# Optimization experiments

Measured on AMD Instinct MI355X. Metric: run time of the kernel, lower is better.

Reference implementation:

```python
import jax, jax.numpy as jnp
import numpy as np

B, SQ, SK, D, H = 8, 2048, 2048, 512, 8
QP, KP, VP = 512, 512, 4096  # VP must equal D*H for O_w to accept the concat


def setup_inputs() -> dict:
    key = jax.random.key(0)
    ks = jax.random.split(key, 9)
    q_in = jax.random.normal(ks[0], (B, SQ, D), dtype=jnp.float32)
    k_in = jax.random.normal(ks[1], (B, SK, D), dtype=jnp.float32)
    v_in = jax.random.normal(ks[2], (B, SK, D), dtype=jnp.float32)
    mask = jax.random.randint(ks[3], (B, SQ, SK), 0, 2, dtype=jnp.int32)
    W_q = jax.random.normal(ks[4], (D, QP), dtype=jnp.float32) * 0.02
    W_k = jax.random.normal(ks[5], (D, KP), dtype=jnp.float32) * 0.02
    W_v = jax.random.normal(ks[6], (D, VP), dtype=jnp.float32) * 0.02
    W_o = jax.random.normal(ks[7], (VP, D), dtype=jnp.float32) * 0.02
    b_o = jnp.zeros((D,), dtype=jnp.float32)
    return {"q_in": q_in, "k_in": k_in, "v_in": v_in,
            "W_q": W_q, "W_k": W_k, "W_v": W_v, "W_o": W_o, "b_o": b_o,
            "mask": mask}


def reference(q_in, k_in, v_in, W_q, W_k, W_v, W_o, b_o, mask):
    b, sq, d = q_in.shape
    sk = k_in.shape[1]
    # NOTE: original scales by sqrt(input_dim // num_heads), NOT actual head dim
    scale = jnp.asarray(np.sqrt(d // H), dtype=q_in.dtype)
    q = q_in @ W_q  # (B, Sq, QP)
    k = k_in @ W_k  # (B, Sk, KP)
    v = v_in @ W_v  # (B, Sk, VP)
    q_h = q.reshape(b, sq, H, -1).transpose(0, 2, 1, 3)  # (B,H,Sq,dq)
    k_h = k.reshape(b, sk, H, -1).transpose(0, 2, 1, 3)  # (B,H,Sk,dk)
    v_h = v.reshape(b, sk, H, -1).transpose(0, 2, 1, 3)  # (B,H,Sk,dv)
    attn = jnp.einsum('bhid,bhkd->bhik', q_h, k_h)  # (B,H,Sq,Sk)
    attn = jnp.where(mask[:, None, :, :] == 0, jnp.asarray(-1e9, attn.dtype), attn)
    attn = jax.nn.softmax(attn / scale, axis=-1)
    out = attn @ v_h  # (B,H,Sq,dv)
    # Faithful to original bug: transpose(0,1) swaps BATCH and HEAD, then reshape
    out = jnp.transpose(out, (1, 0, 2, 3)).reshape(b, sq, -1)  # (B,Sq,H*dv)
    return out @ W_o + b_o
```

## Files before the change

kernel.cpp:

```cpp
#include <hip/hip_runtime.h>
#include <math.h>

typedef __bf16 bf16x8 __attribute__((ext_vector_type(8)));
typedef float fx4 __attribute__((ext_vector_type(4)));
typedef unsigned short u16;
typedef unsigned short u16x8 __attribute__((ext_vector_type(8)));
typedef unsigned int u32;

__device__ __forceinline__ fx4 mfma16(bf16x8 a, bf16x8 b, fx4 c) {
  return __builtin_amdgcn_mfma_f32_16x16x32_bf16(a, b, c, 0, 0, 0);
}
__device__ __forceinline__ u16 f2bf(float f) {
  u32 u = __float_as_uint(f);
  u += 0x7fffu + ((u >> 16) & 1u);
  return (u16)(u >> 16);
}

#define BB 8
#define SS 2048
#define DD 512
#define HH 8
#define DQ 64
#define DV 512
#define VP 4096

#define OFF_QP  ((size_t)0)
#define OFF_KP  ((size_t)16777216)
#define OFF_WQT ((size_t)33554432)
#define OFF_WKT ((size_t)34078720)
#define OFF_WVT ((size_t)34603008)
#define OFF_WOT ((size_t)38797312)
#define OFF_VT  ((size_t)76546048)
#define OFF_XB  ((size_t)210763776)

__global__ __launch_bounds__(256) void transpose_w(const float* __restrict__ W,
                                                   u16* __restrict__ Wt,
                                                   int K, int N) {
  __shared__ float t[32][33];
  const int n0 = blockIdx.x * 32, k0 = blockIdx.y * 32;
  const int tx = threadIdx.x & 31, ty = threadIdx.x >> 5;
#pragma unroll
  for (int i = 0; i < 32; i += 8)
    t[ty + i][tx] = W[(size_t)(k0 + ty + i) * N + n0 + tx];
  __syncthreads();
#pragma unroll
  for (int i = 0; i < 32; i += 8)
    Wt[(size_t)(n0 + ty + i) * K + k0 + tx] = f2bf(t[tx][ty + i]);
}

template <int AFP32, int EPI>
__global__ __launch_bounds__(256) void gemm_bt(const void* __restrict__ Ap,
                                               const u16* __restrict__ Bt,
                                               void* __restrict__ Cp,
                                               int M, int N, int K,
                                               const float* __restrict__ bias,
                                               float scale) {
  __shared__ union {
    struct { u16 As[128 * 32]; u16 Bs[128 * 32]; } s;
    u16 T[4][64 * 68];
  } sm;
  const int tid = threadIdx.x;
  const int lane = tid & 63, w = tid >> 6;
  const int lhi = lane >> 4, llo = lane & 15;
  const int wm = w >> 1, wn = w & 1;
  const int m0 = blockIdx.y * 128, n0 = blockIdx.x * 128;

  fx4 acc[4][4];
#pragma unroll
  for (int i = 0; i < 4; ++i)
#pragma unroll
    for (int j = 0; j < 4; ++j) acc[i][j] = (fx4){0.f, 0.f, 0.f, 0.f};

  for (int k0 = 0; k0 < K; k0 += 32) {
    if (AFP32) {
      const float* A = (const float*)Ap;
      const int row = tid >> 1, co = (tid & 1) * 16;
      const float* src = A + (size_t)(m0 + row) * K + k0 + co;
      float4 v0 = *(const float4*)(src + 0);
      float4 v1 = *(const float4*)(src + 4);
      float4 v2 = *(const float4*)(src + 8);
      float4 v3 = *(const float4*)(src + 12);
      u16x8 p0 = {f2bf(v0.x), f2bf(v0.y), f2bf(v0.z), f2bf(v0.w),
                  f2bf(v1.x), f2bf(v1.y), f2bf(v1.z), f2bf(v1.w)};
      u16x8 p1 = {f2bf(v2.x), f2bf(v2.y), f2bf(v2.z), f2bf(v2.w),
                  f2bf(v3.x), f2bf(v3.y), f2bf(v3.z), f2bf(v3.w)};
      *(u16x8*)&sm.s.As[row * 32 + co] = p0;
      *(u16x8*)&sm.s.As[row * 32 + co + 8] = p1;
    } else {
      const u16* A = (const u16*)Ap;
#pragma unroll
      for (int j = 0; j < 2; ++j) {
        int cc = j * 256 + tid;
        int row = cc >> 2, c8 = (cc & 3) * 8;
        *(uint4*)&sm.s.As[cc * 8] = *(const uint4*)&A[(size_t)(m0 + row) * K + k0 + c8];
      }
    }
#pragma unroll
    for (int j = 0; j < 2; ++j) {
      int cc = j * 256 + tid;
      int row = cc >> 2, c8 = (cc & 3) * 8;
      *(uint4*)&sm.s.Bs[cc * 8] = *(const uint4*)&Bt[(size_t)(n0 + row) * K + k0 + c8];
    }
    __syncthreads();
    bf16x8 af[4], bfv[4];
#pragma unroll
    for (int mi = 0; mi < 4; ++mi)
      af[mi] = *(const bf16x8*)&sm.s.As[(wm * 64 + mi * 16 + llo) * 32 + lhi * 8];
#pragma unroll
    for (int ni = 0; ni < 4; ++ni)
      bfv[ni] = *(const bf16x8*)&sm.s.Bs[(wn * 64 + ni * 16 + llo) * 32 + lhi * 8];
#pragma unroll
    for (int mi = 0; mi < 4; ++mi)
#pragma unroll
      for (int ni = 0; ni < 4; ++ni)
        acc[mi][ni] = mfma16(af[mi], bfv[ni], acc[mi][ni]);
    __syncthreads();
  }

  const int rbase = m0 + wm * 64, cbase = n0 + wn * 64;
  if (EPI == 0) {
    u16* C = (u16*)Cp;
#pragma unroll
    for (int mi = 0; mi < 4; ++mi) {
      int r0 = rbase + mi * 16 + lhi * 4;
#pragma unroll
      for (int ni = 0; ni < 4; ++ni) {
        int c = cbase + ni * 16 + llo;
#pragma unroll
        for (int r = 0; r < 4; ++r)
          C[(size_t)(r0 + r) * N + c] = f2bf(acc[mi][ni][r] * scale);
      }
    }
  } else if (EPI == 1) {
    u16* Tw = &sm.T[w][0];
#pragma unroll
    for (int mi = 0; mi < 4; ++mi)
#pragma unroll
      for (int ni = 0; ni < 4; ++ni) {
        ushort4 pk;
        pk.x = f2bf(acc[mi][ni][0]);
        pk.y = f2bf(acc[mi][ni][1]);
        pk.z = f2bf(acc[mi][ni][2]);
        pk.w = f2bf(acc[mi][ni][3]);
        *(ushort4*)&Tw[(ni * 16 + llo) * 68 + mi * 16 + lhi * 4] = pk;
      }
    u16* VtC = (u16*)Cp;
    const int bsel = rbase >> 11;
    const int sb = rbase & 2047;
    u16* dst = VtC + ((size_t)(bsel * VP + cbase + lane)) * SS + sb;
#pragma unroll
    for (int j = 0; j < 8; ++j) {
      u16x8 vv = *(u16x8*)&Tw[lane * 68 + j * 8];
      *(u16x8*)&dst[j * 8] = vv;
    }
  } else {
    float* C = (float*)Cp;
#pragma unroll
    for (int ni = 0; ni < 4; ++ni) {
      int c = cbase + ni * 16 + llo;
      float bv = bias[c];
#pragma unroll
      for (int mi = 0; mi < 4; ++mi) {
        int r0 = rbase + mi * 16 + lhi * 4;
#pragma unroll
        for (int r = 0; r < 4; ++r)
          C[(size_t)(r0 + r) * N + c] = acc[mi][ni][r] + bv;
      }
    }
  }
}

#define SM_S 68
__global__ __launch_bounds__(256, 2) void attn(const u16* __restrict__ Qp,
                                               const u16* __restrict__ Kp,
                                               const u16* __restrict__ Vt,
                                               const int* __restrict__ mask,
                                               u16* __restrict__ Xb) {
  const int lin = blockIdx.x;
  const int xcd = lin & 7, idx = lin >> 3;
  const int bh = xcd * 8 + (idx >> 5);
  const int qt = idx & 31;
  const int b = bh & 7, h = bh >> 3;
  const int m0 = qt * 64;
  const int tid = threadIdx.x, w = tid >> 6, lane = tid & 63;
  const int lhi = lane >> 4, llo = lane & 15;

  __shared__ float Ssm[64 * SM_S];
  __shared__ u16 Psm[64 * SM_S];
  __shared__ float sm_l[64];

  bf16x8 qf[4][2];
#pragma unroll
  for (int mt = 0; mt < 4; ++mt)
#pragma unroll
    for (int ks = 0; ks < 2; ++ks)
      qf[mt][ks] = *(const bf16x8*)&Qp[(size_t)(b * SS + m0 + mt * 16 + llo) * 512 +
                                       h * DQ + ks * 32 + lhi * 8];

  fx4 acc[4][8];
#pragma unroll
  for (int mt = 0; mt < 4; ++mt)
#pragma unroll
    for (int nt = 0; nt < 8; ++nt) acc[mt][nt] = (fx4){0.f, 0.f, 0.f, 0.f};

  const int r8 = tid >> 3, c8 = (tid & 7) * 8;
  const int* mrow0 = mask + (size_t)(b * SS + m0 + r8) * SS;
  const int* mrow1 = mrow0 + 32 * SS;
  float ls0 = 0.f, ls1 = 0.f;

  const int colw = w * 16 + llo;
  const size_t kbase = (size_t)(b * SS) * 512 + h * DQ + lhi * 8;

  for (int n0 = 0; n0 < SS; n0 += 64) {
    bf16x8 kf0 = *(const bf16x8*)&Kp[kbase + (size_t)(n0 + colw) * 512];
    bf16x8 kf1 = *(const bf16x8*)&Kp[kbase + (size_t)(n0 + colw) * 512 + 32];
    int4 ma0 = *(const int4*)&mrow0[n0 + c8];
    int4 ma1 = *(const int4*)&mrow0[n0 + c8 + 4];
    int4 mb0 = *(const int4*)&mrow1[n0 + c8];
    int4 mb1 = *(const int4*)&mrow1[n0 + c8 + 4];

#pragma unroll
    for (int mt = 0; mt < 4; ++mt) {
      fx4 s = (fx4){0.f, 0.f, 0.f, 0.f};
      s = mfma16(qf[mt][0], kf0, s);
      s = mfma16(qf[mt][1], kf1, s);
#pragma unroll
      for (int r = 0; r < 4; ++r)
        Ssm[(mt * 16 + lhi * 4 + r) * SM_S + colw] = s[r];
    }
    __syncthreads();

#pragma unroll
    for (int half = 0; half < 2; ++half) {
      const int rr = r8 + half * 32;
      const int4 mv0 = half ? mb0 : ma0;
      const int4 mv1 = half ? mb1 : ma1;
      float4 xa = *(const float4*)&Ssm[rr * SM_S + c8];
      float4 xb = *(const float4*)&Ssm[rr * SM_S + c8 + 4];
      float x0 = mv0.x ? xa.x : -1.25e8f;
      float x1 = mv0.y ? xa.y : -1.25e8f;
      float x2 = mv0.z ? xa.z : -1.25e8f;
      float x3 = mv0.w ? xa.w : -1.25e8f;
      float x4 = mv1.x ? xb.x : -1.25e8f;
      float x5 = mv1.y ? xb.y : -1.25e8f;
      float x6 = mv1.z ? xb.z : -1.25e8f;
      float x7 = mv1.w ? xb.w : -1.25e8f;
      float p0 = __expf(x0), p1 = __expf(x1), p2 = __expf(x2), p3 = __expf(x3);
      float p4 = __expf(x4), p5 = __expf(x5), p6 = __expf(x6), p7 = __expf(x7);
      u16x8 pb = {f2bf(p0), f2bf(p1), f2bf(p2), f2bf(p3),
                  f2bf(p4), f2bf(p5), f2bf(p6), f2bf(p7)};
      *(u16x8*)&Psm[rr * SM_S + c8] = pb;
      float ps = ((p0 + p1) + (p2 + p3)) + ((p4 + p5) + (p6 + p7));
      if (half) ls1 += ps; else ls0 += ps;
    }
    __syncthreads();

    bf16x8 pf[4][2];
#pragma unroll
    for (int mt = 0; mt < 4; ++mt)
#pragma unroll
      for (int kk = 0; kk < 2; ++kk)
        pf[mt][kk] = *(const bf16x8*)&Psm[(mt * 16 + llo) * SM_S + kk * 32 + lhi * 8];
#pragma unroll
    for (int nt = 0; nt < 8; ++nt) {
      const size_t vrow =
          (size_t)(b * VP + h * DV + w * 128 + nt * 16 + llo) * SS + n0 + lhi * 8;
      bf16x8 vf0 = *(const bf16x8*)&Vt[vrow];
      bf16x8 vf1 = *(const bf16x8*)&Vt[vrow + 32];
#pragma unroll
      for (int mt = 0; mt < 4; ++mt) {
        fx4 a = acc[mt][nt];
        a = mfma16(pf[mt][0], vf0, a);
        a = mfma16(pf[mt][1], vf1, a);
        acc[mt][nt] = a;
      }
    }
  }

  ls0 += __shfl_xor(ls0, 1); ls0 += __shfl_xor(ls0, 2); ls0 += __shfl_xor(ls0, 4);
  ls1 += __shfl_xor(ls1, 1); ls1 += __shfl_xor(ls1, 2); ls1 += __shfl_xor(ls1, 4);
  if ((tid & 7) == 0) { sm_l[r8] = ls0; sm_l[r8 + 32] = ls1; }
  __syncthreads();

  float linv[4][4];
#pragma unroll
  for (int mt = 0; mt < 4; ++mt)
#pragma unroll
    for (int r = 0; r < 4; ++r) linv[mt][r] = 1.0f / sm_l[mt * 16 + lhi * 4 + r];

  u16* Xs = (u16*)Ssm;
  const int er = tid >> 4, ec = (tid & 15) * 32;
#pragma unroll
  for (int mt = 0; mt < 4; ++mt) {
#pragma unroll
    for (int nt = 0; nt < 8; ++nt)
#pragma unroll
      for (int r = 0; r < 4; ++r)
        Xs[(lhi * 4 + r) * 520 + w * 128 + nt * 16 + llo] =
            f2bf(acc[mt][nt][r] * linv[mt][r]);
    __syncthreads();
    {
      const u16* src = Xs + er * 520 + ec;
      u16* dst = Xb + (size_t)((h * 8 + b) * SS + m0 + mt * 16 + er) * 512 + ec;
      uint4 a0 = *(const uint4*)(src + 0);
      uint4 a1 = *(const uint4*)(src + 8);
      uint4 a2 = *(const uint4*)(src + 16);
      uint4 a3 = *(const uint4*)(src + 24);
      *(uint4*)(dst + 0) = a0;
      *(uint4*)(dst + 8) = a1;
      *(uint4*)(dst + 16) = a2;
      *(uint4*)(dst + 24) = a3;
    }
    __syncthreads();
  }
}

extern "C" void kernel_launch(void* const* d_in, const int* in_sizes, int n_in,
                              void* d_out, int out_size, void* d_ws, size_t ws_size,
                              hipStream_t stream) {
  (void)in_sizes; (void)n_in; (void)out_size; (void)ws_size;
  const float* q_in = (const float*)d_in[0];
  const float* k_in = (const float*)d_in[1];
  const float* v_in = (const float*)d_in[2];
  const float* W_q  = (const float*)d_in[3];
  const float* W_k  = (const float*)d_in[4];
  const float* W_v  = (const float*)d_in[5];
  const float* W_o  = (const float*)d_in[6];
  const float* b_o  = (const float*)d_in[7];
  const int*   mask = (const int*)d_in[8];

  char* ws = (char*)d_ws;
  u16* Qp   = (u16*)(ws + OFF_QP);
  u16* Kp   = (u16*)(ws + OFF_KP);
  u16* Wqt  = (u16*)(ws + OFF_WQT);
  u16* Wkt  = (u16*)(ws + OFF_WKT);
  u16* Wvt  = (u16*)(ws + OFF_WVT);
  u16* Wot  = (u16*)(ws + OFF_WOT);
  u16* Vt   = (u16*)(ws + OFF_VT);
  u16* Xb   = (u16*)(ws + OFF_XB);

  transpose_w<<<dim3(16, 16), 256, 0, stream>>>(W_q, Wqt, 512, 512);
  transpose_w<<<dim3(16, 16), 256, 0, stream>>>(W_k, Wkt, 512, 512);
  transpose_w<<<dim3(128, 16), 256, 0, stream>>>(W_v, Wvt, 512, 4096);
  transpose_w<<<dim3(16, 128), 256, 0, stream>>>(W_o, Wot, 4096, 512);

  gemm_bt<1, 0><<<dim3(4, 128), 256, 0, stream>>>(q_in, Wqt, Qp, 16384, 512, 512, nullptr, 0.125f);
  gemm_bt<1, 0><<<dim3(4, 128), 256, 0, stream>>>(k_in, Wkt, Kp, 16384, 512, 512, nullptr, 1.0f);
  gemm_bt<1, 1><<<dim3(32, 128), 256, 0, stream>>>(v_in, Wvt, Vt, 16384, 4096, 512, nullptr, 1.0f);

  attn<<<dim3(2048), 256, 0, stream>>>(Qp, Kp, Vt, mask, Xb);

  gemm_bt<0, 2><<<dim3(4, 128), 256, 0, stream>>>(Xb, Wot, d_out, 16384, 512, 4096, b_o, 1.0f);
}
```

Before: 1.378 ms.

## Bit-pack transposed mask and fuse exp into score MFMA with prefetch

Adds a pre-pass that packs the int32 mask into per-column 32-bit words so each attention block reads bits instead of the full int mask for every head. The attention kernel now applies the mask and exp directly on MFMA outputs, double-buffers the P tile, holds Q in LDS, and prefetches the next K and mask tile, which removes one barrier and the float score staging. GEMM bf16 operand tiles use global-to-LDS async loads. This costs an extra pack kernel and a 4 MB workspace, and row sums are now reduced per wave through shuffles.

```diff
diff --git a/kernel.cpp b/kernel.cpp
--- a/kernel.cpp
+++ b/kernel.cpp
@@ -15,6 +15,12 @@
   u += 0x7fffu + ((u >> 16) & 1u);
   return (u16)(u >> 16);
 }
+
+#define ASYNC16(gsrc, ldst)                                                        \
+  __builtin_amdgcn_global_load_lds(                                                \
+      (const __attribute__((address_space(1))) unsigned int*)(unsigned long long)(gsrc), \
+      (__attribute__((address_space(3))) unsigned int*)(unsigned int)(unsigned long long)(ldst), \
+      16, 0, 0)
 
 #define BB 8
 #define SS 2048
@@ -30,6 +36,7 @@
 #define OFF_WKT ((size_t)34078720)
 #define OFF_WVT ((size_t)34603008)
 #define OFF_WOT ((size_t)38797312)
+#define OFF_MPT ((size_t)42991616)
 #define OFF_VT  ((size_t)76546048)
 #define OFF_XB  ((size_t)210763776)
 
@@ -46,6 +53,31 @@
 #pragma unroll
   for (int i = 0; i < 32; i += 8)
     Wt[(size_t)(n0 + ty + i) * K + k0 + tx] = f2bf(t[tx][ty + i]);
+}
+
+__global__ __launch_bounds__(256) void pack_mask_t(const int* __restrict__ mask,
+                                                   u32* __restrict__ mpt) {
+  __shared__ int tile[64 * 260];
+  const int b = blockIdx.z, row0 = blockIdx.y * 64, col0 = blockIdx.x * 256;
+  const int tid = threadIdx.x;
+#pragma unroll
+  for (int j = 0; j < 16; ++j) {
+    int idx = j * 1024 + tid * 4;
+    int row = idx >> 8, col = idx & 255;
+    int4 v = *(const int4*)&mask[(size_t)(b * SS + row0 + row) * SS + col0 + col];
+    *(int4*)&tile[row * 260 + col] = v;
+  }
+  __syncthreads();
+  const int col = tid;
+  u32 w0 = 0, w1 = 0;
+#pragma unroll
+  for (int r = 0; r < 32; ++r) {
+    if (tile[r * 260 + col] != 0) w0 |= (1u << r);
+    if (tile[(r + 32) * 260 + col] != 0) w1 |= (1u << r);
+  }
+  size_t base = ((size_t)(b * 64) + (row0 >> 5)) * 2048 + col0 + col;
+  mpt[base] = w0;
+  mpt[base + 2048] = w1;
 }
 
 template <int AFP32, int EPI>
@@ -92,14 +124,16 @@
       for (int j = 0; j < 2; ++j) {
         int cc = j * 256 + tid;
         int row = cc >> 2, c8 = (cc & 3) * 8;
-        *(uint4*)&sm.s.As[cc * 8] = *(const uint4*)&A[(size_t)(m0 + row) * K + k0 + c8];
+        ASYNC16(&A[(size_t)(m0 + row) * K + k0 + c8],
+                (char*)sm.s.As + j * 4096 + w * 1024);
       }
     }
 #pragma unroll
     for (int j = 0; j < 2; ++j) {
       int cc = j * 256 + tid;
       int row = cc >> 2, c8 = (cc & 3) * 8;
-      *(uint4*)&sm.s.Bs[cc * 8] = *(const uint4*)&Bt[(size_t)(n0 + row) * K + k0 + c8];
+      ASYNC16(&Bt[(size_t)(n0 + row) * K + k0 + c8],
+              (char*)sm.s.Bs + j * 4096 + w * 1024);
     }
     __syncthreads();
     bf16x8 af[4], bfv[4];
@@ -170,11 +204,12 @@
   }
 }
 
-#define SM_S 68
+#define PS_ 68
+#define QS_ 72
 __global__ __launch_bounds__(256, 2) void attn(const u16* __restrict__ Qp,
                                                const u16* __restrict__ Kp,
                                                const u16* __restrict__ Vt,
-                                               const int* __restrict__ mask,
+                                               const u32* __restrict__ mpt,
                                                u16* __restrict__ Xb) {
   const int lin = blockIdx.x;
   const int xcd = lin & 7, idx = lin >> 3;
@@ -185,88 +220,80 @@
   const int tid = threadIdx.x, w = tid >> 6, lane = tid & 63;
   const int lhi = lane >> 4, llo = lane & 15;
 
-  __shared__ float Ssm[64 * SM_S];
-  __shared__ u16 Psm[64 * SM_S];
+  __shared__ u16 Qs[64 * QS_];
+  __shared__ u16 Psm[2][64 * PS_];
+  __shared__ float sm_lp[4][64];
   __shared__ float sm_l[64];
 
-  bf16x8 qf[4][2];
+  {
+    int row = tid >> 2, c0 = (tid & 3) * 16;
+    const u16* src = &Qp[(size_t)(b * SS + m0 + row) * 512 + h * DQ + c0];
+    *(uint4*)&Qs[row * QS_ + c0] = *(const uint4*)(src);
+    *(uint4*)&Qs[row * QS_ + c0 + 8] = *(const uint4*)(src + 8);
+  }
+
+  fx4 acc[4][8];
 #pragma unroll
   for (int mt = 0; mt < 4; ++mt)
 #pragma unroll
-    for (int ks = 0; ks < 2; ++ks)
-      qf[mt][ks] = *(const bf16x8*)&Qp[(size_t)(b * SS + m0 + mt * 16 + llo) * 512 +
-                                       h * DQ + ks * 32 + lhi * 8];
-
-  fx4 acc[4][8];
-#pragma unroll
-  for (int mt = 0; mt < 4; ++mt)
-#pragma unroll
     for (int nt = 0; nt < 8; ++nt) acc[mt][nt] = (fx4){0.f, 0.f, 0.f, 0.f};
-
-  const int r8 = tid >> 3, c8 = (tid & 7) * 8;
-  const int* mrow0 = mask + (size_t)(b * SS + m0 + r8) * SS;
-  const int* mrow1 = mrow0 + 32 * SS;
-  float ls0 = 0.f, ls1 = 0.f;
+  fx4 lac[4];
+#pragma unroll
+  for (int mt = 0; mt < 4; ++mt) lac[mt] = (fx4){0.f, 0.f, 0.f, 0.f};
 
   const int colw = w * 16 + llo;
   const size_t kbase = (size_t)(b * SS) * 512 + h * DQ + lhi * 8;
+  const u32* mpt_b = mpt + (size_t)(b * 64 + (m0 >> 5)) * 2048 + colw;
+  const size_t vbase = (size_t)(b * VP + h * DV + w * 128) * SS + lhi * 8;
+
+  bf16x8 kf0 = *(const bf16x8*)&Kp[kbase + (size_t)colw * 512];
+  bf16x8 kf1 = *(const bf16x8*)&Kp[kbase + (size_t)colw * 512 + 32];
+  u32 mw0 = mpt_b[0], mw1 = mpt_b[2048];
+
+  __syncthreads();
 
   for (int n0 = 0; n0 < SS; n0 += 64) {
-    bf16x8 kf0 = *(const bf16x8*)&Kp[kbase + (size_t)(n0 + colw) * 512];
-    bf16x8 kf1 = *(const bf16x8*)&Kp[kbase + (size_t)(n0 + colw) * 512 + 32];
-    int4 ma0 = *(const int4*)&mrow0[n0 + c8];
-    int4 ma1 = *(const int4*)&mrow0[n0 + c8 + 4];
-    int4 mb0 = *(const int4*)&mrow1[n0 + c8];
-    int4 mb1 = *(const int4*)&mrow1[n0 + c8 + 4];
-
+    const int cur = (n0 >> 6) & 1;
+    u16* P = &Psm[cur][0];
 #pragma unroll
     for (int mt = 0; mt < 4; ++mt) {
+      bf16x8 qa0 = *(const bf16x8*)&Qs[(mt * 16 + llo) * QS_ + lhi * 8];
+      bf16x8 qa1 = *(const bf16x8*)&Qs[(mt * 16 + llo) * QS_ + 32 + lhi * 8];
       fx4 s = (fx4){0.f, 0.f, 0.f, 0.f};
-      s = mfma16(qf[mt][0], kf0, s);
-      s = mfma16(qf[mt][1], kf1, s);
-#pragma unroll
-      for (int r = 0; r < 4; ++r)
-        Ssm[(mt * 16 + lhi * 4 + r) * SM_S + colw] = s[r];
-    }
+      s = mfma16(qa0, kf0, s);
+      s = mfma16(qa1, kf1, s);
+      const u32 mwv = (mt < 2) ? mw0 : mw1;
+      const int bb = (mt & 1) * 16 + lhi * 4;
+#pragma unroll
+      for (int r = 0; r < 4; ++r) {
+        float p = ((mwv >> (bb + r)) & 1u) ? __expf(s[r]) : 0.f;
+        lac[mt][r] += p;
+        P[(mt * 16 + lhi * 4 + r) * PS_ + colw] = f2bf(p);
+      }
+    }
+    const int n1 = (n0 + 64) & (SS - 1);
+    kf0 = *(const bf16x8*)&Kp[kbase + (size_t)(n1 + colw) * 512];
+    kf1 = *(const bf16x8*)&Kp[kbase + (size_t)(n1 + colw) * 512 + 32];
+    mw0 = mpt_b[n1];
+    mw1 = mpt_b[n1 + 2048];
+    bf16x8 v00 = *(const bf16x8*)&Vt[vbase + (size_t)llo * SS + n0];
+    bf16x8 v01 = *(const bf16x8*)&Vt[vbase + (size_t)llo * SS + n0 + 32];
     __syncthreads();
 
-#pragma unroll
-    for (int half = 0; half < 2; ++half) {
-      const int rr = r8 + half * 32;
-      const int4 mv0 = half ? mb0 : ma0;
-      const int4 mv1 = half ? mb1 : ma1;
-      float4 xa = *(const float4*)&Ssm[rr * SM_S + c8];
-      float4 xb = *(const float4*)&Ssm[rr * SM_S + c8 + 4];
-      float x0 = mv0.x ? xa.x : -1.25e8f;
-      float x1 = mv0.y ? xa.y : -1.25e8f;
-      float x2 = mv0.z ? xa.z : -1.25e8f;
-      float x3 = mv0.w ? xa.w : -1.25e8f;
-      float x4 = mv1.x ? xb.x : -1.25e8f;
-      float x5 = mv1.y ? xb.y : -1.25e8f;
-      float x6 = mv1.z ? xb.z : -1.25e8f;
-      float x7 = mv1.w ? xb.w : -1.25e8f;
-      float p0 = __expf(x0), p1 = __expf(x1), p2 = __expf(x2), p3 = __expf(x3);
-      float p4 = __expf(x4), p5 = __expf(x5), p6 = __expf(x6), p7 = __expf(x7);
-      u16x8 pb = {f2bf(p0), f2bf(p1), f2bf(p2), f2bf(p3),
-                  f2bf(p4), f2bf(p5), f2bf(p6), f2bf(p7)};
-      *(u16x8*)&Psm[rr * SM_S + c8] = pb;
-      float ps = ((p0 + p1) + (p2 + p3)) + ((p4 + p5) + (p6 + p7));
-      if (half) ls1 += ps; else ls0 += ps;
-    }
-    __syncthreads();
-
     bf16x8 pf[4][2];
 #pragma unroll
     for (int mt = 0; mt < 4; ++mt)
 #pragma unroll
       for (int kk = 0; kk < 2; ++kk)
-        pf[mt][kk] = *(const bf16x8*)&Psm[(mt * 16 + llo) * SM_S + kk * 32 + lhi * 8];
+        pf[mt][kk] = *(const bf16x8*)&P[(mt * 16 + llo) * PS_ + kk * 32 + lhi * 8];
 #pragma unroll
     for (int nt = 0; nt < 8; ++nt) {
-      const size_t vrow =
-          (size_t)(b * VP + h * DV + w * 128 + nt * 16 + llo) * SS + n0 + lhi * 8;
-      bf16x8 vf0 = *(const bf16x8*)&Vt[vrow];
-      bf16x8 vf1 = *(const bf16x8*)&Vt[vrow + 32];
+      bf16x8 vf0, vf1;
+      if (nt == 0) { vf0 = v00; vf1 = v01; }
+      else {
+        vf0 = *(const bf16x8*)&Vt[vbase + (size_t)(nt * 16 + llo) * SS + n0];
+        vf1 = *(const bf16x8*)&Vt[vbase + (size_t)(nt * 16 + llo) * SS + n0 + 32];
+      }
 #pragma unroll
       for (int mt = 0; mt < 4; ++mt) {
         fx4 a = acc[mt][nt];
@@ -277,10 +304,26 @@
     }
   }
 
-  ls0 += __shfl_xor(ls0, 1); ls0 += __shfl_xor(ls0, 2); ls0 += __shfl_xor(ls0, 4);
-  ls1 += __shfl_xor(ls1, 1); ls1 += __shfl_xor(ls1, 2); ls1 += __shfl_xor(ls1, 4);
-  if ((tid & 7) == 0) { sm_l[r8] = ls0; sm_l[r8 + 32] = ls1; }
+#pragma unroll
+  for (int mt = 0; mt < 4; ++mt)
+#pragma unroll
+    for (int r = 0; r < 4; ++r) {
+      float v = lac[mt][r];
+      v += __shfl_xor(v, 1); v += __shfl_xor(v, 2);
+      v += __shfl_xor(v, 4); v += __shfl_xor(v, 8);
+      lac[mt][r] = v;
+    }
+  if (llo == 0) {
+#pragma unroll
+    for (int mt = 0; mt < 4; ++mt)
+#pragma unroll
+      for (int r = 0; r < 4; ++r)
+        sm_lp[w][mt * 16 + lhi * 4 + r] = lac[mt][r];
+  }
   __syncthreads();
+  if (tid < 64)
+    sm_l[tid] = sm_lp[0][tid] + sm_lp[1][tid] + sm_lp[2][tid] + sm_lp[3][tid];
+  __syncthreads();
 
   float linv[4][4];
 #pragma unroll
@@ -288,7 +331,7 @@
 #pragma unroll
     for (int r = 0; r < 4; ++r) linv[mt][r] = 1.0f / sm_l[mt * 16 + lhi * 4 + r];
 
-  u16* Xs = (u16*)Ssm;
+  u16* Xs = &Psm[0][0];
   const int er = tid >> 4, ec = (tid & 15) * 32;
 #pragma unroll
   for (int mt = 0; mt < 4; ++mt) {
@@ -336,6 +379,7 @@
   u16* Wkt  = (u16*)(ws + OFF_WKT);
   u16* Wvt  = (u16*)(ws + OFF_WVT);
   u16* Wot  = (u16*)(ws + OFF_WOT);
+  u32* mpt  = (u32*)(ws + OFF_MPT);
   u16* Vt   = (u16*)(ws + OFF_VT);
   u16* Xb   = (u16*)(ws + OFF_XB);
 
@@ -344,11 +388,13 @@
   transpose_w<<<dim3(128, 16), 256, 0, stream>>>(W_v, Wvt, 512, 4096);
   transpose_w<<<dim3(16, 128), 256, 0, stream>>>(W_o, Wot, 4096, 512);
 
+  pack_mask_t<<<dim3(8, 32, 8), 256, 0, stream>>>(mask, mpt);
+
   gemm_bt<1, 0><<<dim3(4, 128), 256, 0, stream>>>(q_in, Wqt, Qp, 16384, 512, 512, nullptr, 0.125f);
   gemm_bt<1, 0><<<dim3(4, 128), 256, 0, stream>>>(k_in, Wkt, Kp, 16384, 512, 512, nullptr, 1.0f);
   gemm_bt<1, 1><<<dim3(32, 128), 256, 0, stream>>>(v_in, Wvt, Vt, 16384, 4096, 512, nullptr, 1.0f);
 
-  attn<<<dim3(2048), 256, 0, stream>>>(Qp, Kp, Vt, mask, Xb);
+  attn<<<dim3(2048), 256, 0, stream>>>(Qp, Kp, Vt, mpt, Xb);
 
   gemm_bt<0, 2><<<dim3(4, 128), 256, 0, stream>>>(Xb, Wot, d_out, 16384, 512, 4096, b_o, 1.0f);
 }
```

Result: slower. 1.493 ms (+8.3%).
